# Kernel optimization log

Hardware: AMD Instinct MI355X
Metric: run time of the kernel (lower is better)

The kernel has to match this reference:

```python
import jax, jax.numpy as jnp
import numpy as np

DIM = 1024
RANK = 8
POOL = 16
SCALE = 8.0 / 8.0  # alpha / rank


def setup_inputs() -> dict:
    key = jax.random.key(0)
    ks = jax.random.split(key, 8)
    B, N = 8, 4096
    x = jax.random.normal(ks[0], (B, N, DIM), dtype=jnp.float32)
    weight = jax.random.normal(ks[1], (3 * DIM, DIM), dtype=jnp.float32) * 0.02
    bias = jax.random.normal(ks[2], (3 * DIM,), dtype=jnp.float32) * 0.02
    A_q_pool = jax.random.normal(ks[3], (POOL, DIM, RANK), dtype=jnp.float32) * 0.02
    B_q_pool = jax.random.normal(ks[4], (POOL, RANK, DIM), dtype=jnp.float32) * 0.02
    A_v_pool = jax.random.normal(ks[5], (POOL, DIM, RANK), dtype=jnp.float32) * 0.02
    B_v_pool = jax.random.normal(ks[6], (POOL, RANK, DIM), dtype=jnp.float32) * 0.02
    idx = jax.random.randint(ks[7], (B, 1), 0, POOL, dtype=jnp.int64 if jax.config.jax_enable_x64 else jnp.int32)
    frozen_mask = jnp.zeros((POOL,), dtype=bool)
    return {"x": x, "weight": weight, "bias": bias,
            "A_q_pool": A_q_pool, "B_q_pool": B_q_pool,
            "A_v_pool": A_v_pool, "B_v_pool": B_v_pool,
            "idx": idx, "frozen_mask": frozen_mask}


def _maybe_freeze(pool, i, fz):
    g = pool[i]  # [B, ., .] per-sample gather
    return jnp.where(fz, jax.lax.stop_gradient(g), g)


def reference(x, weight, bias, A_q_pool, B_q_pool, A_v_pool, B_v_pool, idx, frozen_mask):
    # Base QKV projection: [B, N, 3*dim]
    qkv = jnp.einsum('bni,oi->bno', x, weight) + bias
    i = idx[:, 0]                      # [B]
    fz = frozen_mask[i][:, None, None]  # [B,1,1]
    A_q = _maybe_freeze(A_q_pool, i, fz)  # [B, dim, rank]
    B_q = _maybe_freeze(B_q_pool, i, fz)  # [B, rank, dim]
    A_v = _maybe_freeze(A_v_pool, i, fz)
    B_v = _maybe_freeze(B_v_pool, i, fz)
    # Low-rank update: (x @ A) @ B, rank-8 bottleneck
    new_q = jnp.einsum('bnr,brj->bnj', jnp.einsum('bni,bir->bnr', x, A_q), B_q)
    new_v = jnp.einsum('bnr,brj->bnj', jnp.einsum('bni,bir->bnr', x, A_v), B_v)
    qkv = qkv.at[:, :, :DIM].add(SCALE * new_q)
    qkv = qkv.at[:, :, -DIM:].add(SCALE * new_v)
    return qkv
```

## Files before the change

### kernel.cpp

```cpp
#include <hip/hip_runtime.h>
#include <hip/hip_bf16.h>
#include <stdint.h>

#define DIM   1024
#define ODIM  3072
#define MROWS 32768
#define RANK  8

typedef unsigned short u16;
typedef __attribute__((ext_vector_type(8))) short short8;
typedef __attribute__((ext_vector_type(8))) unsigned short u16x8;
typedef __attribute__((ext_vector_type(4))) unsigned short u16x4;
typedef __attribute__((ext_vector_type(4))) float f32x4;

__device__ __forceinline__ u16 f2bf(float f) {
    uint32_t u = __float_as_uint(f);
    u += 0x7fffu + ((u >> 16) & 1u);
    return (u16)(u >> 16);
}

__device__ __forceinline__ void gl2lds16(const void* g, void* l) {
    __builtin_amdgcn_global_load_lds(
        (const __attribute__((address_space(1))) void*)(uintptr_t)g,
        (__attribute__((address_space(3))) void*)(uint32_t)(uintptr_t)l,
        16, 0, 0);
}

#define BAR()    do { asm volatile("" ::: "memory"); __builtin_amdgcn_s_barrier(); asm volatile("" ::: "memory"); } while (0)
#define WAITV4() asm volatile("s_waitcnt vmcnt(4)" ::: "memory")
#define WAITV2() asm volatile("s_waitcnt vmcnt(2)" ::: "memory")
#define WAITV0() asm volatile("s_waitcnt vmcnt(0)" ::: "memory")
#define WAITL0() asm volatile("s_waitcnt lgkmcnt(0)" ::: "memory")
#define WAITL8() asm volatile("s_waitcnt lgkmcnt(8)" ::: "memory")
#define SCHED0() __builtin_amdgcn_sched_barrier(0)

__global__ __launch_bounds__(256) void k_convert(const float* __restrict__ src,
                                                 u16* __restrict__ dst, int n) {
    const int stride = gridDim.x * blockDim.x;
    for (int t = blockIdx.x * blockDim.x + threadIdx.x; t * 8 < n; t += stride) {
        const int i = t * 8;
        float4 a = *reinterpret_cast<const float4*>(src + i);
        float4 b = *reinterpret_cast<const float4*>(src + i + 4);
        u16x8 o;
        o[0] = f2bf(a.x); o[1] = f2bf(a.y); o[2] = f2bf(a.z); o[3] = f2bf(a.w);
        o[4] = f2bf(b.x); o[5] = f2bf(b.y); o[6] = f2bf(b.z); o[7] = f2bf(b.w);
        *reinterpret_cast<u16x8*>(dst + i) = o;
    }
}

__global__ __launch_bounds__(256) void k_build(const float* __restrict__ W,
                                               const float* __restrict__ Aq_pool,
                                               const float* __restrict__ Bq_pool,
                                               const float* __restrict__ Av_pool,
                                               const float* __restrict__ Bv_pool,
                                               const int* __restrict__ idx,
                                               u16* __restrict__ Wmq,
                                               u16* __restrict__ Wmv) {
    const int b  = blockIdx.x >> 7;
    const int s  = (blockIdx.x >> 6) & 1;
    const int og = blockIdx.x & 63;
    const int p  = idx[b];
    const float* A  = (s ? Av_pool : Aq_pool) + (size_t)p * DIM * RANK;
    const float* Bp = (s ? Bv_pool : Bq_pool) + (size_t)p * RANK * DIM;
    const float* Ws = W + (size_t)(s ? 2048 : 0) * DIM;
    u16* dst = (s ? Wmv : Wmq) + (size_t)b * DIM * DIM;

    const int t  = threadIdx.x;
    const int i0 = t * 4;
    float a[4][8];
    #pragma unroll
    for (int ii = 0; ii < 4; ++ii) {
        float4 a0 = reinterpret_cast<const float4*>(A + (size_t)(i0 + ii) * RANK)[0];
        float4 a1 = reinterpret_cast<const float4*>(A + (size_t)(i0 + ii) * RANK)[1];
        a[ii][0] = a0.x; a[ii][1] = a0.y; a[ii][2] = a0.z; a[ii][3] = a0.w;
        a[ii][4] = a1.x; a[ii][5] = a1.y; a[ii][6] = a1.z; a[ii][7] = a1.w;
    }
    for (int r = 0; r < 16; ++r) {
        const int o = og * 16 + r;
        float bv[8];
        #pragma unroll
        for (int rr = 0; rr < 8; ++rr) bv[rr] = Bp[(size_t)rr * DIM + o];
        float4 w = *reinterpret_cast<const float4*>(Ws + (size_t)o * DIM + i0);
        float v[4] = {w.x, w.y, w.z, w.w};
        u16x4 ov;
        #pragma unroll
        for (int ii = 0; ii < 4; ++ii) {
            float d = 0.f;
            #pragma unroll
            for (int rr = 0; rr < 8; ++rr) d += a[ii][rr] * bv[rr];
            ov[ii] = f2bf(v[ii] + d);
        }
        *reinterpret_cast<u16x4*>(dst + (size_t)o * DIM + i0) = ov;
    }
}


__device__ __forceinline__ void stage_half(const u16* __restrict__ mat, int row0, int tk,
                                           u16* dst, int wave, int lane) {
    const int lrow = lane >> 3;
    const int g    = (lane & 7) ^ lrow;
    const u16* gp = mat + (size_t)(row0 + wave * 8 + lrow) * DIM + tk + g * 8;
    u16* lp = dst + wave * 8 * 64;
    gl2lds16(gp, lp);
    gl2lds16(gp + (size_t)64 * DIM, lp + 64 * 64);
}

__device__ __forceinline__ void ds_read_A(const u16* sA, int wr, int lane,
                                          int kx0, int kx1, int mh, short8 (&a)[4][2]) {
    #pragma unroll
    for (int f = 0; f < 4; ++f) {
        const int row = wr * 64 + f * 16 + mh * 128 + (lane & 15);
        a[f][0] = *reinterpret_cast<const short8*>(sA + row * 64 + kx0);
        a[f][1] = *reinterpret_cast<const short8*>(sA + row * 64 + kx1);
    }
}
__device__ __forceinline__ void ds_read_B(const u16* sB, int wc, int lane,
                                          int kx0, int kx1, int nh, short8 (&b)[2][2]) {
    #pragma unroll
    for (int f = 0; f < 2; ++f) {
        const int row = wc * 16 + (nh * 2 + f) * 64 + (lane & 15);
        b[f][0] = *reinterpret_cast<const short8*>(sB + row * 64 + kx0);
        b[f][1] = *reinterpret_cast<const short8*>(sB + row * 64 + kx1);
    }
}

template <int MH, int NH>
__device__ __forceinline__ void mfma_quad(const short8 (&a)[4][2], const short8 (&b)[2][2],
                                          f32x4 (&acc)[8][4]) {
    #pragma unroll
    for (int ks = 0; ks < 2; ++ks)
        #pragma unroll
        for (int f = 0; f < 4; ++f)
            #pragma unroll
            for (int g = 0; g < 2; ++g)
                acc[MH * 4 + f][NH * 2 + g] = __builtin_amdgcn_mfma_f32_16x16x32_bf16(
                    a[f][ks], b[g][ks], acc[MH * 4 + f][NH * 2 + g], 0, 0, 0);
}

#define MFMA_BLOCK(MH, NH, AREG, BREG)                  \
    do {                                                \
        BAR();                                          \
        WAITL0();                                       \
        SCHED0();                                       \
        __builtin_amdgcn_s_setprio(1);                  \
        mfma_quad<MH, NH>(AREG, BREG, acc);             \
        __builtin_amdgcn_s_setprio(0);                  \
        SCHED0();                                       \
    } while (0)

__global__ __launch_bounds__(512, 2) void k_gemm(const u16* __restrict__ Xc,
                                                 const u16* __restrict__ Wk,
                                                 const u16* __restrict__ Wmq,
                                                 const u16* __restrict__ Wmv,
                                                 const float* __restrict__ bias,
                                                 float* __restrict__ out) {
    extern __shared__ u16 lds[];
    const int tid  = threadIdx.x;
    const int lane = tid & 63, wave = tid >> 6;
    const int wr = wave >> 2, wc = wave & 3;

    const int orig = blockIdx.x;
    const int wg   = (orig & 7) * 192 + (orig >> 3);
    const int bn   = wg % 12;
    const int bm   = wg / 12;
    const int m0 = bm * 256, n0 = bn * 256;
    const int batch = m0 >> 12;

    const u16* Bmat;
    int nc;
    if (n0 < DIM)           { Bmat = Wmq + (size_t)batch * DIM * DIM; nc = n0; }
    else if (n0 < 2 * DIM)  { Bmat = Wk;                              nc = n0 - DIM; }
    else                    { Bmat = Wmv + (size_t)batch * DIM * DIM; nc = n0 - 2 * DIM; }

    const int kx0 = (((lane >> 4)    ) ^ (lane & 7)) * 8;
    const int kx1 = (((lane >> 4) + 4) ^ (lane & 7)) * 8;

    f32x4 acc[8][4] = {};

    stage_half(Xc,   m0,       0, lds,                    wave, lane);
    stage_half(Bmat, nc,       0, lds + 16384,            wave, lane);
    stage_half(Bmat, nc + 128, 0, lds + 16384 + 128 * 64, wave, lane);
    stage_half(Xc,   m0 + 128, 0, lds + 128 * 64,         wave, lane);
    WAITV0(); BAR();

    #pragma unroll 1
    for (int t = 0; t < 15; ++t) {
        const u16* sA = lds + (t & 1) * 32768;
        const u16* sB = sA + 16384;
        u16* wA = lds + ((t + 1) & 1) * 32768;
        u16* wB = wA + 16384;
        const int tk1 = (t + 1) * 64;
        short8 a_lo[4][2], a_hi[4][2], b0[2][2], b1[2][2];

        ds_read_A(sA, wr, lane, kx0, kx1, 0, a_lo);
        ds_read_B(sB, wc, lane, kx0, kx1, 0, b0);
        stage_half(Xc, m0, tk1, wA, wave, lane);
        WAITL8();
        MFMA_BLOCK(0, 0, a_lo, b0);
        WAITV4(); BAR();

        ds_read_B(sB, wc, lane, kx0, kx1, 1, b1);
        stage_half(Bmat, nc, tk1, wB, wave, lane);
        MFMA_BLOCK(0, 1, a_lo, b1);
        WAITV4(); BAR();

        ds_read_A(sA, wr, lane, kx0, kx1, 1, a_hi);
        stage_half(Bmat, nc + 128, tk1, wB + 128 * 64, wave, lane);
        MFMA_BLOCK(1, 0, a_hi, b0);
        BAR();

        stage_half(Xc, m0 + 128, tk1, wA + 128 * 64, wave, lane);
        MFMA_BLOCK(1, 1, a_hi, b1);
        WAITV4(); BAR();
    }

    {
        const u16* sA = lds + 32768;
        const u16* sB = sA + 16384;
        short8 a_lo[4][2], a_hi[4][2], b0[2][2], b1[2][2];

        ds_read_A(sA, wr, lane, kx0, kx1, 0, a_lo);
        ds_read_B(sB, wc, lane, kx0, kx1, 0, b0);
        WAITL8();
        MFMA_BLOCK(0, 0, a_lo, b0);
        WAITV2(); BAR();

        ds_read_B(sB, wc, lane, kx0, kx1, 1, b1);
        MFMA_BLOCK(0, 1, a_lo, b1);
        WAITV0(); BAR();

        ds_read_A(sA, wr, lane, kx0, kx1, 1, a_hi);
        MFMA_BLOCK(1, 0, a_hi, b0);
        BAR();

        MFMA_BLOCK(1, 1, a_hi, b1);
    }

    const int cn = wc * 16 + (lane & 15);
    float bcol[4];
    #pragma unroll
    for (int ni = 0; ni < 4; ++ni) bcol[ni] = bias[n0 + cn + ni * 64];
    #pragma unroll
    for (int mi = 0; mi < 8; ++mi) {
        const int rb = m0 + wr * 64 + (mi & 3) * 16 + (mi >> 2) * 128 + (lane >> 4) * 4;
        #pragma unroll
        for (int v = 0; v < 4; ++v) {
            const size_t row = (size_t)(rb + v);
            #pragma unroll
            for (int ni = 0; ni < 4; ++ni)
                out[row * ODIM + (size_t)(n0 + cn + ni * 64)] = acc[mi][ni][v] + bcol[ni];
        }
    }
}

extern "C" void kernel_launch(void* const* d_in, const int* in_sizes, int n_in,
                              void* d_out, int out_size, void* d_ws, size_t ws_size,
                              hipStream_t stream) {
    const float* x      = (const float*)d_in[0];
    const float* weight = (const float*)d_in[1];
    const float* bias   = (const float*)d_in[2];
    const float* Aq     = (const float*)d_in[3];
    const float* Bq     = (const float*)d_in[4];
    const float* Av     = (const float*)d_in[5];
    const float* Bv     = (const float*)d_in[6];
    const int*   idx    = (const int*)d_in[7];
    float* out = (float*)d_out;

    u16* Xc  = (u16*)d_ws;
    u16* Wk  = Xc + (size_t)MROWS * DIM;
    u16* Wmq = Wk + (size_t)DIM * DIM;
    u16* Wmv = Wmq + (size_t)8 * DIM * DIM;

    hipFuncSetAttribute(reinterpret_cast<const void*>(k_gemm),
                        hipFuncAttributeMaxDynamicSharedMemorySize, 131072);

    k_convert<<<2048, 256, 0, stream>>>(x, Xc, MROWS * DIM);
    k_convert<<<512, 256, 0, stream>>>(weight + (size_t)DIM * DIM, Wk, DIM * DIM);
    k_build<<<1024, 256, 0, stream>>>(weight, Aq, Bq, Av, Bv, idx, Wmq, Wmv);
    k_gemm<<<1536, 512, 131072, stream>>>(Xc, Wk, Wmq, Wmv, bias, out);
}
```

Measured before the change: 298.2 us.

## Switch GEMM to 32x32x16 MFMA tiles and fold Wk conversion into build kernel

The main GEMM now uses 32x32x16 bf16 MFMA instructions in place of 16x16x32. Fragment loads from LDS are restructured around 32-row fragments, and the epilogue store mapping is rewritten to match the larger accumulator layout. The larger instruction needs fewer issues and fewer LDS fragment reads per unit of work. Separately, conversion of the K-projection weight is merged into the k_build launch as extra blocks, which removes one kernel launch. The new LDS read pattern may cause bank conflicts against the existing XOR swizzle, and the epilogue store pattern changes.

Result: slower. 318.8 us (+6.9%).

```diff
diff --git a/kernel.cpp b/kernel.cpp
--- a/kernel.cpp
+++ b/kernel.cpp
@@ -11,7 +11,7 @@
 typedef __attribute__((ext_vector_type(8))) short short8;
 typedef __attribute__((ext_vector_type(8))) unsigned short u16x8;
 typedef __attribute__((ext_vector_type(4))) unsigned short u16x4;
-typedef __attribute__((ext_vector_type(4))) float f32x4;
+typedef __attribute__((ext_vector_type(16))) float f32x16;
 
 __device__ __forceinline__ u16 f2bf(float f) {
     uint32_t u = __float_as_uint(f);
@@ -55,7 +55,20 @@
                                                const float* __restrict__ Bv_pool,
                                                const int* __restrict__ idx,
                                                u16* __restrict__ Wmq,
-                                               u16* __restrict__ Wmv) {
+                                               u16* __restrict__ Wmv,
+                                               u16* __restrict__ Wk) {
+    if (blockIdx.x >= 1024) {
+        const int bb = blockIdx.x - 1024;
+        const int i = (bb * 256 + threadIdx.x) * 8;
+        const float* src = W + (size_t)DIM * DIM + i;
+        float4 a = *reinterpret_cast<const float4*>(src);
+        float4 b = *reinterpret_cast<const float4*>(src + 4);
+        u16x8 o;
+        o[0] = f2bf(a.x); o[1] = f2bf(a.y); o[2] = f2bf(a.z); o[3] = f2bf(a.w);
+        o[4] = f2bf(b.x); o[5] = f2bf(b.y); o[6] = f2bf(b.z); o[7] = f2bf(b.w);
+        *reinterpret_cast<u16x8*>(Wk + i) = o;
+        return;
+    }
     const int b  = blockIdx.x >> 7;
     const int s  = (blockIdx.x >> 6) & 1;
     const int og = blockIdx.x & 63;
@@ -105,47 +118,31 @@
     gl2lds16(gp + (size_t)64 * DIM, lp + 64 * 64);
 }
 
-__device__ __forceinline__ void ds_read_A(const u16* sA, int wr, int lane,
-                                          int kx0, int kx1, int mh, short8 (&a)[4][2]) {
-    #pragma unroll
-    for (int f = 0; f < 4; ++f) {
-        const int row = wr * 64 + f * 16 + mh * 128 + (lane & 15);
-        a[f][0] = *reinterpret_cast<const short8*>(sA + row * 64 + kx0);
-        a[f][1] = *reinterpret_cast<const short8*>(sA + row * 64 + kx1);
-    }
-}
-__device__ __forceinline__ void ds_read_B(const u16* sB, int wc, int lane,
-                                          int kx0, int kx1, int nh, short8 (&b)[2][2]) {
-    #pragma unroll
-    for (int f = 0; f < 2; ++f) {
-        const int row = wc * 16 + (nh * 2 + f) * 64 + (lane & 15);
-        b[f][0] = *reinterpret_cast<const short8*>(sB + row * 64 + kx0);
-        b[f][1] = *reinterpret_cast<const short8*>(sB + row * 64 + kx1);
-    }
-}
-
-template <int MH, int NH>
-__device__ __forceinline__ void mfma_quad(const short8 (&a)[4][2], const short8 (&b)[2][2],
-                                          f32x4 (&acc)[8][4]) {
-    #pragma unroll
-    for (int ks = 0; ks < 2; ++ks)
-        #pragma unroll
-        for (int f = 0; f < 4; ++f)
-            #pragma unroll
-            for (int g = 0; g < 2; ++g)
-                acc[MH * 4 + f][NH * 2 + g] = __builtin_amdgcn_mfma_f32_16x16x32_bf16(
-                    a[f][ks], b[g][ks], acc[MH * 4 + f][NH * 2 + g], 0, 0, 0);
-}
-
-#define MFMA_BLOCK(MH, NH, AREG, BREG)                  \
-    do {                                                \
-        BAR();                                          \
-        WAITL0();                                       \
-        SCHED0();                                       \
-        __builtin_amdgcn_s_setprio(1);                  \
-        mfma_quad<MH, NH>(AREG, BREG, acc);             \
-        __builtin_amdgcn_s_setprio(0);                  \
-        SCHED0();                                       \
+__device__ __forceinline__ void ds_read_frag(const u16* base, int r0, int lane,
+                                             short8 (&v)[4]) {
+    const int row = r0 + (lane & 31);
+    const int x7  = lane & 7;
+    const int kb  = lane >> 5;
+    #pragma unroll
+    for (int ks = 0; ks < 4; ++ks)
+        v[ks] = *reinterpret_cast<const short8*>(base + row * 64 + ((2 * ks + kb) ^ x7) * 8);
+}
+
+#define MFMA_QUAD(MH, NH, A0, A1, BREG)                                           \
+    do {                                                                          \
+        BAR();                                                                    \
+        WAITL0();                                                                 \
+        SCHED0();                                                                 \
+        __builtin_amdgcn_s_setprio(1);                                            \
+        _Pragma("unroll")                                                         \
+        for (int ks = 0; ks < 4; ++ks) {                                          \
+            acc[2 * MH][NH]     = __builtin_amdgcn_mfma_f32_32x32x16_bf16(        \
+                A0[ks], BREG[ks], acc[2 * MH][NH], 0, 0, 0);                      \
+            acc[2 * MH + 1][NH] = __builtin_amdgcn_mfma_f32_32x32x16_bf16(        \
+                A1[ks], BREG[ks], acc[2 * MH + 1][NH], 0, 0, 0);                  \
+        }                                                                         \
+        __builtin_amdgcn_s_setprio(0);                                            \
+        SCHED0();                                                                 \
     } while (0)
 
 __global__ __launch_bounds__(512, 2) void k_gemm(const u16* __restrict__ Xc,
@@ -172,10 +169,7 @@
     else if (n0 < 2 * DIM)  { Bmat = Wk;                              nc = n0 - DIM; }
     else                    { Bmat = Wmv + (size_t)batch * DIM * DIM; nc = n0 - 2 * DIM; }
 
-    const int kx0 = (((lane >> 4)    ) ^ (lane & 7)) * 8;
-    const int kx1 = (((lane >> 4) + 4) ^ (lane & 7)) * 8;
-
-    f32x4 acc[8][4] = {};
+    f32x16 acc[4][2] = {};
 
     stage_half(Xc,   m0,       0, lds,                    wave, lane);
     stage_half(Bmat, nc,       0, lds + 16384,            wave, lane);
@@ -190,65 +184,72 @@
         u16* wA = lds + ((t + 1) & 1) * 32768;
         u16* wB = wA + 16384;
         const int tk1 = (t + 1) * 64;
-        short8 a_lo[4][2], a_hi[4][2], b0[2][2], b1[2][2];
-
-        ds_read_A(sA, wr, lane, kx0, kx1, 0, a_lo);
-        ds_read_B(sB, wc, lane, kx0, kx1, 0, b0);
+        short8 f0[4], f1[4], f2[4], f3[4], g0[4], g1[4];
+
+        ds_read_frag(sA, wr * 64,       lane, f0);
+        ds_read_frag(sA, wr * 64 + 32,  lane, f1);
+        ds_read_frag(sB, wc * 32,       lane, g0);
         stage_half(Xc, m0, tk1, wA, wave, lane);
         WAITL8();
-        MFMA_BLOCK(0, 0, a_lo, b0);
+        MFMA_QUAD(0, 0, f0, f1, g0);
         WAITV4(); BAR();
 
-        ds_read_B(sB, wc, lane, kx0, kx1, 1, b1);
+        ds_read_frag(sB, wc * 32 + 128, lane, g1);
         stage_half(Bmat, nc, tk1, wB, wave, lane);
-        MFMA_BLOCK(0, 1, a_lo, b1);
+        MFMA_QUAD(0, 1, f0, f1, g1);
         WAITV4(); BAR();
 
-        ds_read_A(sA, wr, lane, kx0, kx1, 1, a_hi);
+        ds_read_frag(sA, wr * 64 + 128, lane, f2);
+        ds_read_frag(sA, wr * 64 + 160, lane, f3);
         stage_half(Bmat, nc + 128, tk1, wB + 128 * 64, wave, lane);
-        MFMA_BLOCK(1, 0, a_hi, b0);
+        MFMA_QUAD(1, 0, f2, f3, g0);
         BAR();
 
         stage_half(Xc, m0 + 128, tk1, wA + 128 * 64, wave, lane);
-        MFMA_BLOCK(1, 1, a_hi, b1);
+        MFMA_QUAD(1, 1, f2, f3, g1);
         WAITV4(); BAR();
     }
 
     {
         const u16* sA = lds + 32768;
         const u16* sB = sA + 16384;
-        short8 a_lo[4][2], a_hi[4][2], b0[2][2], b1[2][2];
-
-        ds_read_A(sA, wr, lane, kx0, kx1, 0, a_lo);
-        ds_read_B(sB, wc, lane, kx0, kx1, 0, b0);
+        short8 f0[4], f1[4], f2[4], f3[4], g0[4], g1[4];
+
+        ds_read_frag(sA, wr * 64,       lane, f0);
+        ds_read_frag(sA, wr * 64 + 32,  lane, f1);
+        ds_read_frag(sB, wc * 32,       lane, g0);
         WAITL8();
-        MFMA_BLOCK(0, 0, a_lo, b0);
+        MFMA_QUAD(0, 0, f0, f1, g0);
         WAITV2(); BAR();
 
-        ds_read_B(sB, wc, lane, kx0, kx1, 1, b1);
-        MFMA_BLOCK(0, 1, a_lo, b1);
+        ds_read_frag(sB, wc * 32 + 128, lane, g1);
+        MFMA_QUAD(0, 1, f0, f1, g1);
         WAITV0(); BAR();
 
-        ds_read_A(sA, wr, lane, kx0, kx1, 1, a_hi);
-        MFMA_BLOCK(1, 0, a_hi, b0);
+        ds_read_frag(sA, wr * 64 + 128, lane, f2);
+        ds_read_frag(sA, wr * 64 + 160, lane, f3);
+        MFMA_QUAD(1, 0, f2, f3, g0);
         BAR();
 
-        MFMA_BLOCK(1, 1, a_hi, b1);
-    }
-
-    const int cn = wc * 16 + (lane & 15);
-    float bcol[4];
-    #pragma unroll
-    for (int ni = 0; ni < 4; ++ni) bcol[ni] = bias[n0 + cn + ni * 64];
-    #pragma unroll
-    for (int mi = 0; mi < 8; ++mi) {
-        const int rb = m0 + wr * 64 + (mi & 3) * 16 + (mi >> 2) * 128 + (lane >> 4) * 4;
+        MFMA_QUAD(1, 1, f2, f3, g1);
+    }
+
+    const int cb = lane & 31;
+    const int rv = 4 * (lane >> 5);
+    float bcol[2];
+    #pragma unroll
+    for (int G = 0; G < 2; ++G) bcol[G] = bias[n0 + wc * 32 + G * 128 + cb];
+    #pragma unroll
+    for (int F = 0; F < 4; ++F) {
+        const int rbase = m0 + wr * 64 + (F & 1) * 32 + (F >> 1) * 128 + rv;
         #pragma unroll
-        for (int v = 0; v < 4; ++v) {
-            const size_t row = (size_t)(rb + v);
+        for (int G = 0; G < 2; ++G) {
+            const size_t col = (size_t)(n0 + wc * 32 + G * 128 + cb);
             #pragma unroll
-            for (int ni = 0; ni < 4; ++ni)
-                out[row * ODIM + (size_t)(n0 + cn + ni * 64)] = acc[mi][ni][v] + bcol[ni];
+            for (int v = 0; v < 16; ++v) {
+                const size_t row = (size_t)(rbase + (v & 3) + 8 * (v >> 2));
+                out[row * ODIM + col] = acc[F][G][v] + bcol[G];
+            }
         }
     }
 }
@@ -275,7 +276,6 @@
                         hipFuncAttributeMaxDynamicSharedMemorySize, 131072);
 
     k_convert<<<2048, 256, 0, stream>>>(x, Xc, MROWS * DIM);
-    k_convert<<<512, 256, 0, stream>>>(weight + (size_t)DIM * DIM, Wk, DIM * DIM);
-    k_build<<<1024, 256, 0, stream>>>(weight, Aq, Bq, Av, Bv, idx, Wmq, Wmv);
+    k_build<<<1536, 256, 0, stream>>>(weight, Aq, Bq, Av, Bv, idx, Wmq, Wmv, Wk);
     k_gemm<<<1536, 512, 131072, stream>>>(Xc, Wk, Wmq, Wmv, bias, out);
 }
```
